# Performance work log

Measured on AMD Instinct MI355X. Metric: run time of the kernel, lower is better.

The kernel has to match this reference:

```python
import jax, jax.numpy as jnp
import numpy as np
import math

D_MODEL = 1024
N_HEADS = 16
D_K = D_MODEL // N_HEADS


def setup_inputs() -> dict:
    key = jax.random.key(0)
    ks = jax.random.split(key, 5)
    std = math.sqrt(2.0 / (D_MODEL + D_MODEL))
    x = jax.random.normal(ks[0], (2, 2048, D_MODEL), dtype=jnp.float32)
    W_q = jax.random.normal(ks[1], (D_MODEL, D_MODEL), dtype=jnp.float32) * std
    W_k = jax.random.normal(ks[2], (D_MODEL, D_MODEL), dtype=jnp.float32) * std
    W_v = jax.random.normal(ks[3], (D_MODEL, D_MODEL), dtype=jnp.float32) * std
    W_o = jax.random.normal(ks[4], (D_MODEL, D_MODEL), dtype=jnp.float32) * std
    return {"x": x, "W_q": W_q, "W_k": W_k, "W_v": W_v, "W_o": W_o}


def reference(x, W_q, W_k, W_v, W_o):
    B, S, D = x.shape
    H, dk = N_HEADS, D_K
    # projections: (B,S,D) @ (D,D)
    def split_heads(t):  # (B,S,D) -> (B,H,S,dk)
        return t.reshape(B, S, H, dk).transpose(0, 2, 1, 3)
    Q = split_heads(x @ W_q)
    K = split_heads(x @ W_k)
    V = split_heads(x @ W_v)
    scale = 1.0 / math.sqrt(dk)
    scores = jnp.einsum("bhqd,bhkd->bhqk", Q, K) * scale  # (B,H,S,S)
    attn = jax.nn.softmax(scores, axis=-1)
    out = jnp.einsum("bhqk,bhkd->bhqd", attn, V)  # (B,H,S,dk)
    concat = out.transpose(0, 2, 1, 3).reshape(B, S, D)
    return concat @ W_o
```

## Files before the change

kernel.cpp:

```cpp
#include <hip/hip_runtime.h>
#include <hip/hip_bf16.h>
#include <math.h>

#define DMODEL 1024
#define NHEADS 16
#define DKH    64
#define BATCH  2
#define SEQ    2048
#define MROWS  (BATCH * SEQ)
#define LOG2E  1.4426950408889634f

typedef __bf16 bf16_t;
typedef bf16_t bf16x8 __attribute__((ext_vector_type(8)));
typedef bf16_t bf16x4 __attribute__((ext_vector_type(4)));
typedef float  floatx4 __attribute__((ext_vector_type(4)));

__device__ __forceinline__ void glds16(const bf16_t* g, bf16_t* l) {
    __builtin_amdgcn_global_load_lds((__attribute__((address_space(1))) unsigned*)(g),
                                     (__attribute__((address_space(3))) unsigned*)(l),
                                     16, 0, 0);
}

__global__ void cast_x_kernel(const float* __restrict__ x, bf16_t* __restrict__ xb) {
    int i = (blockIdx.x * 256 + threadIdx.x) * 4;
    float4 v = *(const float4*)(x + i);
    bf16_t o0 = (bf16_t)v.x, o1 = (bf16_t)v.y, o2 = (bf16_t)v.z, o3 = (bf16_t)v.w;
    bf16_t o[4] = {o0, o1, o2, o3};
    *(uint2*)(xb + i) = *(uint2*)o;
}

__global__ void transpose4_kernel(const float* __restrict__ W0, const float* __restrict__ W1,
                                  const float* __restrict__ W2, const float* __restrict__ W3,
                                  bf16_t* __restrict__ Wt) {
    __shared__ float t[32][33];
    const float* W = (blockIdx.z == 0) ? W0 : (blockIdx.z == 1) ? W1 : (blockIdx.z == 2) ? W2 : W3;
    bf16_t* dst = Wt + (size_t)blockIdx.z * DMODEL * DMODEL;
    int bx = blockIdx.x, by = blockIdx.y;
    int tx = threadIdx.x, ty = threadIdx.y;
#pragma unroll
    for (int i = 0; i < 32; i += 8)
        t[ty + i][tx] = W[(size_t)(by * 32 + ty + i) * DMODEL + bx * 32 + tx];
    __syncthreads();
#pragma unroll
    for (int i = 0; i < 32; i += 8)
        dst[(size_t)(bx * 32 + ty + i) * DMODEL + by * 32 + tx] = (bf16_t)t[tx][ty + i];
}

template<int MODE>
__global__ __launch_bounds__(256) void gemm128_kernel(const bf16_t* __restrict__ A,
                                                      const bf16_t* __restrict__ Bt,
                                                      void* __restrict__ outp) {
    __shared__ bf16_t As[128 * 64];
    __shared__ bf16_t Bs[128 * 64];
    int tid = threadIdx.x;
    int w = tid >> 6, l = tid & 63, g = l >> 4, lm = l & 15;
    int wr = w >> 1, wc = w & 1;
    int m0 = blockIdx.y * 128, n0 = blockIdx.x * 128;
    int r8 = l >> 3, s8 = l & 7, cw = s8 ^ r8;

    floatx4 acc[4][4];
#pragma unroll
    for (int i = 0; i < 4; ++i)
#pragma unroll
        for (int j = 0; j < 4; ++j) { floatx4 z = {0.f, 0.f, 0.f, 0.f}; acc[i][j] = z; }

    const bf16_t* Ag = A  + (size_t)(m0 + w * 32 + r8) * DMODEL + cw * 8;
    const bf16_t* Bg = Bt + (size_t)(n0 + w * 32 + r8) * DMODEL + cw * 8;

    for (int k0 = 0; k0 < DMODEL; k0 += 64) {
        __syncthreads();
#pragma unroll
        for (int j = 0; j < 4; ++j) {
            glds16(Ag + (size_t)j * 8 * DMODEL + k0, &As[(w * 32 + j * 8) * 64]);
            glds16(Bg + (size_t)j * 8 * DMODEL + k0, &Bs[(w * 32 + j * 8) * 64]);
        }
        __syncthreads();
#pragma unroll
        for (int kk = 0; kk < 2; ++kk) {
            bf16x8 af[4], bfr[4];
            int c = kk * 4 + g;
            int sw = (c ^ (lm & 7)) * 8;
#pragma unroll
            for (int i = 0; i < 4; ++i) {
                af[i]  = *(const bf16x8*)&As[(wr * 64 + i * 16 + lm) * 64 + sw];
                bfr[i] = *(const bf16x8*)&Bs[(wc * 64 + i * 16 + lm) * 64 + sw];
            }
#pragma unroll
            for (int i = 0; i < 4; ++i)
#pragma unroll
                for (int j = 0; j < 4; ++j)
                    acc[i][j] = __builtin_amdgcn_mfma_f32_16x16x32_bf16(af[i], bfr[j], acc[i][j], 0, 0, 0);
        }
    }

    const size_t NX = (size_t)MROWS * DMODEL;
#pragma unroll
    for (int i = 0; i < 4; ++i) {
#pragma unroll
        for (int j = 0; j < 4; ++j) {
            int nc = n0 + wc * 64 + j * 16 + lm;
            int mb = m0 + wr * 64 + i * 16 + g * 4;
            if (MODE == 0) {
                int mat = n0 >> 10;
                int col = nc & 1023;
                int hh = col >> 6, d = col & 63;
                int b = mb >> 11;
                int bh2 = b * NHEADS + hh;
                int s0 = mb & 2047;
                int kt = s0 >> 6;
                bf16_t* base = (bf16_t*)outp;
                if (mat == 0) {
#pragma unroll
                    for (int r = 0; r < 4; ++r)
                        base[((size_t)bh2 * SEQ + s0 + r) * DKH + d] = (bf16_t)(acc[i][j][r] * (0.125f * LOG2E));
                } else if (mat == 1) {
                    int kk = d >> 5, gK = (d >> 3) & 3, jK = d & 7;
                    int rt = s0 & 63, mt = rt >> 4, lmK = rt & 15;
                    bf16_t* Kfb = base + NX;
                    size_t tb = (((size_t)bh2 * 32 + kt) * 8 + mt * 2 + kk) * 512 + (gK * 16 + lmK) * 8 + jK;
#pragma unroll
                    for (int r = 0; r < 4; ++r)
                        Kfb[tb + (size_t)r * 8] = (bf16_t)acc[i][j][r];
                } else {
                    int dt = d >> 4, lmV = d & 15;
                    int s63 = s0 & 63;
                    int kkV = s63 >> 5, gV = (s63 >> 3) & 3, jV = s63 & 7;
                    bf16_t* Vfb = base + 2 * NX;
                    size_t tb = (((size_t)bh2 * 32 + kt) * 8 + dt * 2 + kkV) * 512 + (gV * 16 + lmV) * 8 + jV;
                    bf16x4 pk = {(bf16_t)acc[i][j][0], (bf16_t)acc[i][j][1],
                                 (bf16_t)acc[i][j][2], (bf16_t)acc[i][j][3]};
                    *(bf16x4*)&Vfb[tb] = pk;
                }
            } else {
#pragma unroll
                for (int r = 0; r < 4; ++r)
                    ((float*)outp)[(size_t)(mb + r) * DMODEL + nc] = acc[i][j][r];
            }
        }
    }
}

__global__ __launch_bounds__(256, 2) void attn_kernel(const bf16_t* __restrict__ Q,
                                                      const bf16_t* __restrict__ Kf,
                                                      const bf16_t* __restrict__ Vf,
                                                      bf16_t* __restrict__ Cc) {
    __shared__ __align__(16) char smem[32768];
    bf16_t* Ps = (bf16_t*)smem;
    float*  Ms = (float*)smem;

    int tid = threadIdx.x;
    int w = tid >> 6, l = tid & 63, g = l >> 4, lm = l & 15;
    int qw = w & 1, ks = w >> 1;
    int bh = blockIdx.x, b = bh >> 4, h = bh & 15;
    int q0 = blockIdx.y * 128 + qw * 64;
    int xsw = lm & 14;

    const bf16_t* Qh  = Q  + ((size_t)bh * SEQ + q0) * DKH;
    const bf16_t* Kfh = Kf + (size_t)bh * 32 * 8 * 512 + l * 8;
    const bf16_t* Vfh = Vf + (size_t)bh * 32 * 8 * 512 + l * 8;

    bf16x8 qf[4][2];
#pragma unroll
    for (int nt = 0; nt < 4; ++nt)
#pragma unroll
        for (int kk = 0; kk < 2; ++kk)
            qf[nt][kk] = *(const bf16x8*)(Qh + (size_t)(nt * 16 + lm) * DKH + kk * 32 + g * 8);

    floatx4 oacc[4][4];
#pragma unroll
    for (int dt = 0; dt < 4; ++dt)
#pragma unroll
        for (int nt = 0; nt < 4; ++nt) { floatx4 z = {0.f, 0.f, 0.f, 0.f}; oacc[dt][nt] = z; }
    float lsum[4] = {0.f, 0.f, 0.f, 0.f};

    int kt0 = ks * 16;
    bf16x8 kf[4][2], kfn[4][2], vf[4][2];
#pragma unroll
    for (int mt = 0; mt < 4; ++mt)
#pragma unroll
        for (int kk = 0; kk < 2; ++kk)
            kf[mt][kk] = *(const bf16x8*)(Kfh + ((size_t)kt0 * 8 + mt * 2 + kk) * 512);

#pragma unroll 2
    for (int it = 0; it < 16; ++it) {
        int kt = kt0 + it;
        const bf16_t* Vt = Vfh + (size_t)kt * 8 * 512;

#pragma unroll
        for (int dt = 0; dt < 4; ++dt)
#pragma unroll
            for (int kk = 0; kk < 2; ++kk)
                vf[dt][kk] = *(const bf16x8*)(Vt + (dt * 2 + kk) * 512);

        floatx4 sacc[4][4];
#pragma unroll
        for (int mt = 0; mt < 4; ++mt)
#pragma unroll
            for (int nt = 0; nt < 4; ++nt) { floatx4 z = {0.f, 0.f, 0.f, 0.f}; sacc[mt][nt] = z; }
#pragma unroll
        for (int kk = 0; kk < 2; ++kk)
#pragma unroll
            for (int mt = 0; mt < 4; ++mt)
#pragma unroll
                for (int nt = 0; nt < 4; ++nt)
                    sacc[mt][nt] = __builtin_amdgcn_mfma_f32_16x16x32_bf16(kf[mt][kk], qf[nt][kk], sacc[mt][nt], 0, 0, 0);

        int ktn = (it < 15) ? kt + 1 : kt0;
        const bf16_t* Kn = Kfh + (size_t)ktn * 8 * 512;
#pragma unroll
        for (int mt = 0; mt < 4; ++mt)
#pragma unroll
            for (int kk = 0; kk < 2; ++kk)
                kfn[mt][kk] = *(const bf16x8*)(Kn + (mt * 2 + kk) * 512);

#pragma unroll
        for (int mt = 0; mt < 4; ++mt)
#pragma unroll
            for (int nt = 0; nt < 4; ++nt) {
                float p0 = __builtin_amdgcn_exp2f(sacc[mt][nt][0]);
                float p1 = __builtin_amdgcn_exp2f(sacc[mt][nt][1]);
                float p2 = __builtin_amdgcn_exp2f(sacc[mt][nt][2]);
                float p3 = __builtin_amdgcn_exp2f(sacc[mt][nt][3]);
                lsum[nt] += (p0 + p1) + (p2 + p3);
                bf16x4 pk = {(bf16_t)p0, (bf16_t)p1, (bf16_t)p2, (bf16_t)p3};
                *(bf16x4*)&Ps[w * 4096 + (nt * 16 + lm) * 64 + (((mt * 4 + g) ^ xsw) << 2)] = pk;
            }

#pragma unroll
        for (int kk = 0; kk < 2; ++kk) {
            bf16x8 bp[4];
#pragma unroll
            for (int nt = 0; nt < 4; ++nt)
                bp[nt] = *(const bf16x8*)&Ps[w * 4096 + (nt * 16 + lm) * 64 + (((kk * 8 + g * 2) ^ xsw) << 2)];
#pragma unroll
            for (int dt = 0; dt < 4; ++dt)
#pragma unroll
                for (int nt = 0; nt < 4; ++nt)
                    oacc[dt][nt] = __builtin_amdgcn_mfma_f32_16x16x32_bf16(vf[dt][kk], bp[nt], oacc[dt][nt], 0, 0, 0);
        }

#pragma unroll
        for (int mt = 0; mt < 4; ++mt)
#pragma unroll
            for (int kk = 0; kk < 2; ++kk)
                kf[mt][kk] = kfn[mt][kk];
    }

#pragma unroll
    for (int nt = 0; nt < 4; ++nt) {
        float s = lsum[nt];
        s += __shfl_xor(s, 16, 64);
        s += __shfl_xor(s, 32, 64);
        lsum[nt] = s;
    }

    float linv[4];
#pragma unroll
    for (int pass = 0; pass < 2; ++pass) {
        __syncthreads();
        if (ks == 1) {
#pragma unroll
            for (int dh = 0; dh < 2; ++dh) {
                int dt = pass * 2 + dh;
#pragma unroll
                for (int nt = 0; nt < 4; ++nt)
                    *(floatx4*)&Ms[(qw * 64 + nt * 16 + lm) * 36 + dh * 16 + g * 4] = oacc[dt][nt];
            }
            if (pass == 0 && g == 0)
#pragma unroll
                for (int nt = 0; nt < 4; ++nt)
                    Ms[(qw * 64 + nt * 16 + lm) * 36 + 32] = lsum[nt];
        }
        __syncthreads();
        if (ks == 0) {
            if (pass == 0)
#pragma unroll
                for (int nt = 0; nt < 4; ++nt)
                    linv[nt] = 1.0f / (lsum[nt] + Ms[(qw * 64 + nt * 16 + lm) * 36 + 32]);
#pragma unroll
            for (int dh = 0; dh < 2; ++dh) {
                int dt = pass * 2 + dh;
#pragma unroll
                for (int nt = 0; nt < 4; ++nt) {
                    floatx4 part = *(const floatx4*)&Ms[(qw * 64 + nt * 16 + lm) * 36 + dh * 16 + g * 4];
                    bf16x4 pk = {(bf16_t)((oacc[dt][nt][0] + part[0]) * linv[nt]),
                                 (bf16_t)((oacc[dt][nt][1] + part[1]) * linv[nt]),
                                 (bf16_t)((oacc[dt][nt][2] + part[2]) * linv[nt]),
                                 (bf16_t)((oacc[dt][nt][3] + part[3]) * linv[nt])};
                    int q = q0 + nt * 16 + lm;
                    int d = h * DKH + dt * 16 + g * 4;
                    *(bf16x4*)&Cc[((size_t)(b * SEQ + q)) * DMODEL + d] = pk;
                }
            }
        }
    }
}

extern "C" void kernel_launch(void* const* d_in, const int* in_sizes, int n_in,
                              void* d_out, int out_size, void* d_ws, size_t ws_size,
                              hipStream_t stream) {
    const float* x  = (const float*)d_in[0];
    const float* Wq = (const float*)d_in[1];
    const float* Wk = (const float*)d_in[2];
    const float* Wv = (const float*)d_in[3];
    const float* Wo = (const float*)d_in[4];

    const size_t NX = (size_t)MROWS * DMODEL;
    const size_t NW = (size_t)DMODEL * DMODEL;
    bf16_t* ws  = (bf16_t*)d_ws;
    bf16_t* xb  = ws;
    bf16_t* Wt  = xb + NX;
    bf16_t* Wto = Wt + 3 * NW;
    bf16_t* Qb  = Wt + 4 * NW;
    bf16_t* Kfb = Qb + NX;
    bf16_t* Vfb = Kfb + NX;
    bf16_t* Cc  = Vfb + NX;

    cast_x_kernel<<<NX / 1024, 256, 0, stream>>>(x, xb);
    transpose4_kernel<<<dim3(32, 32, 4), dim3(32, 8), 0, stream>>>(Wq, Wk, Wv, Wo, Wt);

    gemm128_kernel<0><<<dim3(3 * DMODEL / 128, MROWS / 128), 256, 0, stream>>>(xb, Wt, Qb);

    attn_kernel<<<dim3(BATCH * NHEADS, SEQ / 128), 256, 0, stream>>>(Qb, Kfb, Vfb, Cc);

    gemm128_kernel<3><<<dim3(DMODEL / 128, MROWS / 128), 256, 0, stream>>>(Cc, Wto, (float*)d_out);
}
```

Before: 197.9 us.

## Split attention keys four ways per block and add smaller-tile output GEMM

```diff
diff --git a/kernel.cpp b/kernel.cpp
--- a/kernel.cpp
+++ b/kernel.cpp
@@ -140,19 +140,79 @@
     }
 }
 
-__global__ __launch_bounds__(256, 2) void attn_kernel(const bf16_t* __restrict__ Q,
+__global__ __launch_bounds__(256) void gemmO_kernel(const bf16_t* __restrict__ A,
+                                                    const bf16_t* __restrict__ Bt,
+                                                    float* __restrict__ outp) {
+    __shared__ bf16_t As[64 * 64];
+    __shared__ bf16_t Bs[128 * 64];
+    int tid = threadIdx.x;
+    int w = tid >> 6, l = tid & 63, g = l >> 4, lm = l & 15;
+    int wr = w & 1, wc = w >> 1;
+    int m0 = blockIdx.y * 64, n0 = blockIdx.x * 128;
+    int r8 = l >> 3, s8 = l & 7, cw = s8 ^ r8;
+
+    floatx4 acc[2][4];
+#pragma unroll
+    for (int i = 0; i < 2; ++i)
+#pragma unroll
+        for (int j = 0; j < 4; ++j) { floatx4 z = {0.f, 0.f, 0.f, 0.f}; acc[i][j] = z; }
+
+    const bf16_t* Ag = A  + (size_t)(m0 + w * 16 + r8) * DMODEL + cw * 8;
+    const bf16_t* Bg = Bt + (size_t)(n0 + w * 32 + r8) * DMODEL + cw * 8;
+
+    for (int k0 = 0; k0 < DMODEL; k0 += 64) {
+        __syncthreads();
+#pragma unroll
+        for (int j = 0; j < 2; ++j)
+            glds16(Ag + (size_t)j * 8 * DMODEL + k0, &As[(w * 16 + j * 8) * 64]);
+#pragma unroll
+        for (int j = 0; j < 4; ++j)
+            glds16(Bg + (size_t)j * 8 * DMODEL + k0, &Bs[(w * 32 + j * 8) * 64]);
+        __syncthreads();
+#pragma unroll
+        for (int kk = 0; kk < 2; ++kk) {
+            bf16x8 af[2], bfr[4];
+            int c = kk * 4 + g;
+            int sw = (c ^ (lm & 7)) * 8;
+#pragma unroll
+            for (int i = 0; i < 2; ++i)
+                af[i] = *(const bf16x8*)&As[(wr * 32 + i * 16 + lm) * 64 + sw];
+#pragma unroll
+            for (int j = 0; j < 4; ++j)
+                bfr[j] = *(const bf16x8*)&Bs[(wc * 64 + j * 16 + lm) * 64 + sw];
+#pragma unroll
+            for (int i = 0; i < 2; ++i)
+#pragma unroll
+                for (int j = 0; j < 4; ++j)
+                    acc[i][j] = __builtin_amdgcn_mfma_f32_16x16x32_bf16(af[i], bfr[j], acc[i][j], 0, 0, 0);
+        }
+    }
+
+#pragma unroll
+    for (int i = 0; i < 2; ++i)
+#pragma unroll
+        for (int j = 0; j < 4; ++j) {
+            int nc = n0 + wc * 64 + j * 16 + lm;
+            int mb = m0 + wr * 32 + i * 16 + g * 4;
+#pragma unroll
+            for (int r = 0; r < 4; ++r)
+                outp[(size_t)(mb + r) * DMODEL + nc] = acc[i][j][r];
+        }
+}
+
+__global__ __launch_bounds__(256, 4) void attn_kernel(const bf16_t* __restrict__ Q,
                                                       const bf16_t* __restrict__ Kf,
                                                       const bf16_t* __restrict__ Vf,
                                                       bf16_t* __restrict__ Cc) {
-    __shared__ __align__(16) char smem[32768];
-    bf16_t* Ps = (bf16_t*)smem;
-    float*  Ms = (float*)smem;
+    __shared__ __align__(16) char smem[37888];
+    bf16_t* Ps   = (bf16_t*)smem;
+    float*  Mbuf = (float*)smem;
+    float*  Lbuf = (float*)(smem + 36864);
 
     int tid = threadIdx.x;
     int w = tid >> 6, l = tid & 63, g = l >> 4, lm = l & 15;
-    int qw = w & 1, ks = w >> 1;
     int bh = blockIdx.x, b = bh >> 4, h = bh & 15;
-    int q0 = blockIdx.y * 128 + qw * 64;
+    int q0 = blockIdx.y * 64;
     int xsw = lm & 14;
 
     const bf16_t* Qh  = Q  + ((size_t)bh * SEQ + q0) * DKH;
@@ -173,7 +233,7 @@
         for (int nt = 0; nt < 4; ++nt) { floatx4 z = {0.f, 0.f, 0.f, 0.f}; oacc[dt][nt] = z; }
     float lsum[4] = {0.f, 0.f, 0.f, 0.f};
 
-    int kt0 = ks * 16;
+    int kt0 = w * 8;
     bf16x8 kf[4][2], kfn[4][2], vf[4][2];
 #pragma unroll
     for (int mt = 0; mt < 4; ++mt)
@@ -182,7 +242,7 @@
             kf[mt][kk] = *(const bf16x8*)(Kfh + ((size_t)kt0 * 8 + mt * 2 + kk) * 512);
 
 #pragma unroll 2
-    for (int it = 0; it < 16; ++it) {
+    for (int it = 0; it < 8; ++it) {
         int kt = kt0 + it;
         const bf16_t* Vt = Vfh + (size_t)kt * 8 * 512;
 
@@ -205,7 +265,7 @@
                 for (int nt = 0; nt < 4; ++nt)
                     sacc[mt][nt] = __builtin_amdgcn_mfma_f32_16x16x32_bf16(kf[mt][kk], qf[nt][kk], sacc[mt][nt], 0, 0, 0);
 
-        int ktn = (it < 15) ? kt + 1 : kt0;
+        int ktn = (it < 7) ? kt + 1 : kt0;
         const bf16_t* Kn = Kfh + (size_t)ktn * 8 * 512;
 #pragma unroll
         for (int mt = 0; mt < 4; ++mt)
@@ -254,44 +314,40 @@
         lsum[nt] = s;
     }
 
-    float linv[4];
-#pragma unroll
-    for (int pass = 0; pass < 2; ++pass) {
-        __syncthreads();
-        if (ks == 1) {
-#pragma unroll
-            for (int dh = 0; dh < 2; ++dh) {
-                int dt = pass * 2 + dh;
-#pragma unroll
-                for (int nt = 0; nt < 4; ++nt)
-                    *(floatx4*)&Ms[(qw * 64 + nt * 16 + lm) * 36 + dh * 16 + g * 4] = oacc[dt][nt];
-            }
-            if (pass == 0 && g == 0)
-#pragma unroll
-                for (int nt = 0; nt < 4; ++nt)
-                    Ms[(qw * 64 + nt * 16 + lm) * 36 + 32] = lsum[nt];
-        }
-        __syncthreads();
-        if (ks == 0) {
-            if (pass == 0)
-#pragma unroll
-                for (int nt = 0; nt < 4; ++nt)
-                    linv[nt] = 1.0f / (lsum[nt] + Ms[(qw * 64 + nt * 16 + lm) * 36 + 32]);
-#pragma unroll
-            for (int dh = 0; dh < 2; ++dh) {
-                int dt = pass * 2 + dh;
-#pragma unroll
-                for (int nt = 0; nt < 4; ++nt) {
-                    floatx4 part = *(const floatx4*)&Ms[(qw * 64 + nt * 16 + lm) * 36 + dh * 16 + g * 4];
-                    bf16x4 pk = {(bf16_t)((oacc[dt][nt][0] + part[0]) * linv[nt]),
-                                 (bf16_t)((oacc[dt][nt][1] + part[1]) * linv[nt]),
-                                 (bf16_t)((oacc[dt][nt][2] + part[2]) * linv[nt]),
-                                 (bf16_t)((oacc[dt][nt][3] + part[3]) * linv[nt])};
-                    int q = q0 + nt * 16 + lm;
-                    int d = h * DKH + dt * 16 + g * 4;
-                    *(bf16x4*)&Cc[((size_t)(b * SEQ + q)) * DMODEL + d] = pk;
-                }
-            }
+    float linv = 0.f;
+#pragma unroll
+    for (int p = 0; p < 2; ++p) {
+        __syncthreads();
+#pragma unroll
+        for (int dh = 0; dh < 2; ++dh) {
+            int dt = p * 2 + dh;
+#pragma unroll
+            for (int nt = 0; nt < 4; ++nt)
+                *(floatx4*)&Mbuf[w * 2304 + (nt * 16 + lm) * 36 + dh * 16 + g * 4] = oacc[dt][nt];
+        }
+        if (p == 0 && g == 0)
+#pragma unroll
+            for (int nt = 0; nt < 4; ++nt)
+                Lbuf[w * 64 + nt * 16 + lm] = lsum[nt];
+        __syncthreads();
+        if (p == 0) {
+            float lt = 0.f;
+#pragma unroll
+            for (int w2 = 0; w2 < 4; ++w2)
+                lt += Lbuf[w2 * 64 + w * 16 + lm];
+            linv = 1.0f / lt;
+        }
+#pragma unroll
+        for (int cc = 0; cc < 2; ++cc) {
+            floatx4 s = {0.f, 0.f, 0.f, 0.f};
+#pragma unroll
+            for (int w2 = 0; w2 < 4; ++w2)
+                s += *(const floatx4*)&Mbuf[w2 * 2304 + (w * 16 + lm) * 36 + cc * 16 + g * 4];
+            bf16x4 pk = {(bf16_t)(s[0] * linv), (bf16_t)(s[1] * linv),
+                         (bf16_t)(s[2] * linv), (bf16_t)(s[3] * linv)};
+            int q = q0 + w * 16 + lm;
+            int d = h * DKH + p * 32 + cc * 16 + g * 4;
+            *(bf16x4*)&Cc[((size_t)(b * SEQ + q)) * DMODEL + d] = pk;
         }
     }
 }
@@ -321,7 +377,7 @@
 
     gemm128_kernel<0><<<dim3(3 * DMODEL / 128, MROWS / 128), 256, 0, stream>>>(xb, Wt, Qb);
 
-    attn_kernel<<<dim3(BATCH * NHEADS, SEQ / 128), 256, 0, stream>>>(Qb, Kfb, Vfb, Cc);
-
-    gemm128_kernel<3><<<dim3(DMODEL / 128, MROWS / 128), 256, 0, stream>>>(Cc, Wto, (float*)d_out);
-}
+    attn_kernel<<<dim3(BATCH * NHEADS, SEQ / 64), 256, 0, stream>>>(Qb, Kfb, Vfb, Cc);
+
+    gemmO_kernel<<<dim3(DMODEL / 128, MROWS / 64), 256, 0, stream>>>(Cc, Wto, (float*)d_out);
+}
```

Result: slower. 454.7 us (+129.8%).
